# Kernel optimization log

Hardware: AMD Instinct MI355X
Metric: run time of the kernel (lower is better)

## Reference

```python
import jax, jax.numpy as jnp
from jax import lax
import numpy as np

WIN = 11
SIGMA = 1.5
C1 = 0.01 ** 2  # (K1 * data_range)^2 with data_range=1.0
C2 = 0.03 ** 2


def _gaussian_window(channels: int) -> jnp.ndarray:
    coords = np.arange(WIN, dtype=np.float32) - (WIN - 1) / 2.0
    g = np.exp(-(coords ** 2) / (2.0 * SIGMA ** 2))
    g /= g.sum()
    w2d = np.outer(g, g).astype(np.float32)  # [11,11]
    # OIHW depthwise kernel: [C, 1, 11, 11]
    return jnp.asarray(np.tile(w2d[None, None], (channels, 1, 1, 1)))


def _dwconv(x, w, channels):
    pad = WIN // 2
    return lax.conv_general_dilated(
        x, w, window_strides=(1, 1), padding=[(pad, pad), (pad, pad)],
        dimension_numbers=("NCHW", "OIHW", "NCHW"),
        feature_group_count=channels)


def setup_inputs() -> dict:
    key = jax.random.key(0)
    k1, k2 = jax.random.split(key)
    shape = (16, 3, 512, 512)
    pred = jax.random.uniform(k1, shape, dtype=jnp.float32)
    target = jax.random.uniform(k2, shape, dtype=jnp.float32)
    return {"pred": pred, "target": target}


def reference(pred, target):
    C = pred.shape[1]
    w = _gaussian_window(C).astype(pred.dtype)
    # Stack the five fields along batch so a single depthwise conv computes
    # all local windowed statistics in one pass (fused-stat formulation).
    B = pred.shape[0]
    stacked = jnp.concatenate(
        [pred, target, pred * pred, target * target, pred * target], axis=0)
    stats = _dwconv(stacked, w, C)
    mu1, mu2, e_x2, e_y2, e_xy = (
        stats[0:B], stats[B:2 * B], stats[2 * B:3 * B],
        stats[3 * B:4 * B], stats[4 * B:5 * B])
    mu1_sq = mu1 * mu1
    mu2_sq = mu2 * mu2
    mu1_mu2 = mu1 * mu2
    sigma1_sq = e_x2 - mu1_sq
    sigma2_sq = e_y2 - mu2_sq
    sigma12 = e_xy - mu1_mu2
    ssim_map = ((2.0 * mu1_mu2 + C1) * (2.0 * sigma12 + C2)) / (
        (mu1_sq + mu2_sq + C1) * (sigma1_sq + sigma2_sq + C2))
    return jnp.mean(ssim_map)  # size_average=True
```

## Files before the change

### kernel.cpp

```cpp
#include <hip/hip_runtime.h>
#include <math.h>

#define IMG   512
#define NIMG  48
#define TB    64
#define TC    32
#define SR    74
#define PITCH 77
#define STS   (TC * PITCH)
#define C1v   1.0e-4f
#define C2v   9.0e-4f

struct Win { float w[11]; };

template<bool GUARD>
__device__ __forceinline__ void phaseA_unit(
        float2* __restrict__ hs2,
        const float* __restrict__ P,
        const float* __restrict__ T,
        const Win& win, int bx, int y0, int x0, int u) {
    const int r  = u >> 3;
    const int cb = u & 7;
    const int gy = y0 - 5 + r;
    const float* __restrict__ Prow = P + (long)gy * IMG;
    const float* __restrict__ Trow = T + (long)gy * IMG;
    const bool yok = (!GUARD) || ((gy >= 0) & (gy < IMG));

    float s1[4], s2[4], q1[4], q2[4];
    #pragma unroll
    for (int i = 0; i < 4; ++i) { s1[i]=0.f; s2[i]=0.f; q1[i]=0.f; q2[i]=0.f; }

    #pragma unroll
    for (int k = 0; k < 5; ++k) {
        float4 p = make_float4(0.f, 0.f, 0.f, 0.f);
        float4 t = make_float4(0.f, 0.f, 0.f, 0.f);
        bool zero = false;
        if (GUARD)
            zero = (!yok) | ((bx == 0)  & (cb + k <= 1))
                          | ((bx == 15) & (cb + k >= 10));
        if (!zero) {
            const int gx = x0 + 4 * (cb + k - 2);
            p = *(const float4*)(Prow + gx);
            t = *(const float4*)(Trow + gx);
        }
        const float pv[4] = { p.x, p.y, p.z, p.w };
        const float tv[4] = { t.x, t.y, t.z, t.w };
        #pragma unroll
        for (int j4 = 0; j4 < 4; ++j4) {
            const int w = 4 * k + j4;
            if (w >= 3 && w <= 16) {
                const float sm = pv[j4] + tv[j4];
                const float dm = pv[j4] - tv[j4];
                const float sq = sm * sm;
                const float dq = dm * dm;
                #pragma unroll
                for (int i = 0; i < 4; ++i) {
                    const int j = w - 3 - i;
                    if (j >= 0 && j < 11) {
                        const float wj = win.w[j];
                        s1[i] += wj * sm;
                        s2[i] += wj * dm;
                        q1[i] += wj * sq;
                        q2[i] += wj * dq;
                    }
                }
            }
        }
    }
    const int ebase = (4 * cb) * PITCH + r;
    #pragma unroll
    for (int i = 0; i < 4; ++i) {
        hs2[ebase + i * PITCH]       = make_float2(s1[i], s2[i]);
        hs2[STS + ebase + i * PITCH] = make_float2(q1[i], q2[i]);
    }
}

__global__ __launch_bounds__(512, 8) void ssim_kernel(
        const float* __restrict__ pred,
        const float* __restrict__ targ,
        float* __restrict__ partial, Win win) {
    __shared__ float2 hs2[2 * STS];
    __shared__ float wavesum[8];

    const int tid = threadIdx.x;
    const int n   = blockIdx.z;
    const int by  = blockIdx.y;
    const int bx  = blockIdx.x;
    const int y0  = by * TB;
    const int x0  = bx * TC;

    const float* __restrict__ P = pred + (size_t)n * IMG * IMG;
    const float* __restrict__ T = targ + (size_t)n * IMG * IMG;

    const bool guard = (bx == 0) | (bx == 15) | (by == 0) | (by == (IMG / TB - 1));
    if (guard) {
        #pragma unroll 1
        for (int u = tid; u < SR * 8; u += 512)
            phaseA_unit<true >(hs2, P, T, win, bx, y0, x0, u);
    } else {
        #pragma unroll 1
        for (int u = tid; u < SR * 8; u += 512)
            phaseA_unit<false>(hs2, P, T, win, bx, y0, x0, u);
    }
    __syncthreads();

    const int x  = tid & 31;
    const int rg = tid >> 5;
    const int r0 = rg * 4;
    const float2* __restrict__ csd = &hs2[x * PITCH + r0];
    const float2* __restrict__ cqq = &hs2[STS + x * PITCH + r0];

    float sum[4][4];
    #pragma unroll
    for (int st = 0; st < 4; ++st)
        #pragma unroll
        for (int k = 0; k < 4; ++k) sum[st][k] = 0.f;

    #pragma unroll
    for (int m = 0; m < 14; ++m) {
        const float2 sd = csd[m];
        const float2 qq = cqq[m];
        #pragma unroll
        for (int k = 0; k < 4; ++k) {
            const int j = m - k;
            if (j >= 0 && j < 11) {
                const float wj = win.w[j];
                sum[0][k] += wj * sd.x;
                sum[1][k] += wj * sd.y;
                sum[2][k] += wj * qq.x;
                sum[3][k] += wj * qq.y;
            }
        }
    }

    float acc = 0.f;
    #pragma unroll
    for (int k = 0; k < 4; ++k) {
        const float S1 = sum[0][k];
        const float S2 = sum[1][k];
        const float Q1 = sum[2][k];
        const float Q2 = sum[3][k];
        const float s1q = S1 * S1;
        const float s2q = S2 * S2;
        const float A_  = 0.5f * (s1q + s2q);
        const float B_  = 0.5f * (s1q - s2q);
        const float sps = 0.5f * (Q1 + Q2) - A_;
        const float sxx = 0.5f * (Q1 - Q2) - B_;
        const float num = (B_ + C1v) * (sxx + C2v);
        const float den = (A_ + C1v) * (sps + C2v);
        acc += num * __builtin_amdgcn_rcpf(den);
    }

    #pragma unroll
    for (int off = 32; off > 0; off >>= 1)
        acc += __shfl_down(acc, off, 64);
    const int wv = tid >> 6;
    if ((tid & 63) == 0) wavesum[wv] = acc;
    __syncthreads();
    if (tid == 0) {
        float s = 0.f;
        #pragma unroll
        for (int i = 0; i < 8; ++i) s += wavesum[i];
        const int bid = (blockIdx.z * gridDim.y + blockIdx.y) * gridDim.x + blockIdx.x;
        partial[bid] = s;
    }
}

__global__ __launch_bounds__(512) void ssim_reduce_kernel(
        const float* __restrict__ partial,
        float* __restrict__ out,
        int nchunk4, double inv_n) {
    __shared__ double wsum[8];
    const float4* __restrict__ p4 = (const float4*)partial;
    double s = 0.0;
    #pragma unroll 1
    for (int i = threadIdx.x; i < nchunk4; i += 512) {
        const float4 v = p4[i];
        s += (double)((v.x + v.y) + (v.z + v.w));
    }
    #pragma unroll
    for (int off = 32; off > 0; off >>= 1)
        s += __shfl_down(s, off, 64);
    const int wv = threadIdx.x >> 6;
    if ((threadIdx.x & 63) == 0) wsum[wv] = s;
    __syncthreads();
    if (threadIdx.x == 0) {
        double tot = 0.0;
        #pragma unroll
        for (int i = 0; i < 8; ++i) tot += wsum[i];
        out[0] = (float)(tot * inv_n);
    }
}

extern "C" void kernel_launch(void* const* d_in, const int* in_sizes, int n_in,
                              void* d_out, int out_size, void* d_ws, size_t ws_size,
                              hipStream_t stream) {
    const float* pred = (const float*)d_in[0];
    const float* targ = (const float*)d_in[1];
    float* out     = (float*)d_out;
    float* partial = (float*)d_ws;

    Win win;
    {
        double v[11], s = 0.0;
        for (int i = 0; i < 11; ++i) {
            float d   = (float)i - 5.0f;
            float arg = -(d * d) / 4.5f;
            v[i] = exp((double)arg);
            s += v[i];
        }
        for (int i = 0; i < 11; ++i) win.w[i] = (float)(v[i] / s);
    }

    dim3 grid(IMG / TC, IMG / TB, NIMG);
    ssim_kernel<<<grid, 512, 0, stream>>>(pred, targ, partial, win);

    const int nblk = (IMG / TC) * (IMG / TB) * NIMG;
    const double inv_n = 1.0 / ((double)NIMG * IMG * IMG);
    ssim_reduce_kernel<<<1, 512, 0, stream>>>(partial, out, nblk / 4, inv_n);
}
```

Before: 55.10 us.

## Rebalance horizontal pass and split vertical pass by plane with shuffle exchange

The horizontal pass is split into a main phase where each of the 512 threads handles one of the first 64 rows. A tail phase spreads the remaining 10 halo rows over 20 lanes per wave at two output columns each, which removes the strided second loop iteration that left most threads idle. The vertical pass now has each thread handle one plane (sum/diff or squares) for 8 output rows over an 18-tap window. The partner plane is swapped in with a cross-half-wave shuffle, and each half computes the SSIM epilogue for 4 of the 8 rows. This cuts repeated vertical-window LDS reads and balances work, at the cost of shuffle traffic and more registers.

```diff
diff --git a/kernel.cpp b/kernel.cpp
--- a/kernel.cpp
+++ b/kernel.cpp
@@ -14,17 +14,17 @@
 struct Win { float w[11]; };
 
 template<bool GUARD>
-__device__ __forceinline__ void phaseA_unit(
+__device__ __forceinline__ void phaseA_main(
         float2* __restrict__ hs2,
         const float* __restrict__ P,
         const float* __restrict__ T,
-        const Win& win, int bx, int y0, int x0, int u) {
-    const int r  = u >> 3;
-    const int cb = u & 7;
+        const Win& win, int bx, int y0, int x0, int tid) {
+    const int r  = tid >> 3;
+    const int cb = tid & 7;
     const int gy = y0 - 5 + r;
     const float* __restrict__ Prow = P + (long)gy * IMG;
     const float* __restrict__ Trow = T + (long)gy * IMG;
-    const bool yok = (!GUARD) || ((gy >= 0) & (gy < IMG));
+    const bool yok = (!GUARD) || (gy >= 0);
 
     float s1[4], s2[4], q1[4], q2[4];
     #pragma unroll
@@ -75,6 +75,88 @@
     }
 }
 
+template<bool GUARD>
+__device__ __forceinline__ void phaseA_tail(
+        float2* __restrict__ hs2,
+        const float* __restrict__ P,
+        const float* __restrict__ T,
+        const Win& win, int bx, int y0, int x0, int tid) {
+    const int wv = tid >> 6;
+    const int l  = tid & 63;
+    if (l >= 20) return;
+    const int u   = wv * 20 + l;
+    const int r   = 64 + (u >> 4);
+    const int cb2 = u & 15;
+    const int cb  = cb2 >> 1;
+    const int h   = cb2 & 1;
+    const int gy  = y0 - 5 + r;
+    const float* __restrict__ Prow = P + (long)gy * IMG;
+    const float* __restrict__ Trow = T + (long)gy * IMG;
+    const bool yok = (!GUARD) || (gy < IMG);
+    const int lo = 3 - 2 * h;
+
+    float pa[16], pb[16];
+    #pragma unroll
+    for (int k = 0; k < 4; ++k) {
+        const int q = cb + h + k;
+        float4 p = make_float4(0.f, 0.f, 0.f, 0.f);
+        float4 t = make_float4(0.f, 0.f, 0.f, 0.f);
+        bool zero = false;
+        if (GUARD)
+            zero = (!yok) | ((bx == 0)  & (q <= 1))
+                          | ((bx == 15) & (q >= 10));
+        if (!zero) {
+            const int gx = x0 + 4 * (q - 2);
+            p = *(const float4*)(Prow + gx);
+            t = *(const float4*)(Trow + gx);
+        }
+        pa[4*k+0] = p.x; pa[4*k+1] = p.y; pa[4*k+2] = p.z; pa[4*k+3] = p.w;
+        pb[4*k+0] = t.x; pb[4*k+1] = t.y; pb[4*k+2] = t.z; pb[4*k+3] = t.w;
+    }
+
+    float s1[2], s2[2], q1[2], q2[2];
+    #pragma unroll
+    for (int c = 0; c < 2; ++c) { s1[c]=0.f; s2[c]=0.f; q1[c]=0.f; q2[c]=0.f; }
+    #pragma unroll
+    for (int m = 0; m < 12; ++m) {
+        const float a  = pa[lo + m];
+        const float b  = pb[lo + m];
+        const float sm = a + b;
+        const float dm = a - b;
+        const float sq = sm * sm;
+        const float dq = dm * dm;
+        #pragma unroll
+        for (int c = 0; c < 2; ++c) {
+            const int j = m - c;
+            if (j >= 0 && j < 11) {
+                const float wj = win.w[j];
+                s1[c] += wj * sm;
+                s2[c] += wj * dm;
+                q1[c] += wj * sq;
+                q2[c] += wj * dq;
+            }
+        }
+    }
+    #pragma unroll
+    for (int c = 0; c < 2; ++c) {
+        const int C = 4 * cb + 2 * h + c;
+        hs2[C * PITCH + r]       = make_float2(s1[c], s2[c]);
+        hs2[STS + C * PITCH + r] = make_float2(q1[c], q2[c]);
+    }
+}
+
+__device__ __forceinline__ float ssim_epilogue(float S1, float S2, float Q1, float Q2) {
+    const float s1q = S1 * S1;
+    const float s2q = S2 * S2;
+    const float A_  = 0.5f * (s1q + s2q);
+    const float B_  = 0.5f * (s1q - s2q);
+    const float sps = 0.5f * (Q1 + Q2) - A_;
+    const float sxx = 0.5f * (Q1 - Q2) - B_;
+    const float num = (B_ + C1v) * (sxx + C2v);
+    const float den = (A_ + C1v) * (sps + C2v);
+    return num * __builtin_amdgcn_rcpf(den);
+}
+
 __global__ __launch_bounds__(512, 8) void ssim_kernel(
         const float* __restrict__ pred,
         const float* __restrict__ targ,
@@ -94,61 +176,54 @@
 
     const bool guard = (bx == 0) | (bx == 15) | (by == 0) | (by == (IMG / TB - 1));
     if (guard) {
-        #pragma unroll 1
-        for (int u = tid; u < SR * 8; u += 512)
-            phaseA_unit<true >(hs2, P, T, win, bx, y0, x0, u);
+        phaseA_main<true >(hs2, P, T, win, bx, y0, x0, tid);
+        phaseA_tail<true >(hs2, P, T, win, bx, y0, x0, tid);
     } else {
-        #pragma unroll 1
-        for (int u = tid; u < SR * 8; u += 512)
-            phaseA_unit<false>(hs2, P, T, win, bx, y0, x0, u);
+        phaseA_main<false>(hs2, P, T, win, bx, y0, x0, tid);
+        phaseA_tail<false>(hs2, P, T, win, bx, y0, x0, tid);
     }
     __syncthreads();
 
     const int x  = tid & 31;
-    const int rg = tid >> 5;
-    const int r0 = rg * 4;
-    const float2* __restrict__ csd = &hs2[x * PITCH + r0];
-    const float2* __restrict__ cqq = &hs2[STS + x * PITCH + r0];
-
-    float sum[4][4];
-    #pragma unroll
-    for (int st = 0; st < 4; ++st)
-        #pragma unroll
-        for (int k = 0; k < 4; ++k) sum[st][k] = 0.f;
-
-    #pragma unroll
-    for (int m = 0; m < 14; ++m) {
-        const float2 sd = csd[m];
-        const float2 qq = cqq[m];
-        #pragma unroll
-        for (int k = 0; k < 4; ++k) {
+    const int pl = (tid >> 5) & 1;
+    const int ro = tid >> 6;
+    const int r0 = ro * 8;
+    const float2* __restrict__ cp = &hs2[pl * STS + x * PITCH + r0];
+
+    float A0[8], A1[8];
+    #pragma unroll
+    for (int k = 0; k < 8; ++k) { A0[k] = 0.f; A1[k] = 0.f; }
+
+    #pragma unroll
+    for (int m = 0; m < 18; ++m) {
+        const float2 v = cp[m];
+        #pragma unroll
+        for (int k = 0; k < 8; ++k) {
             const int j = m - k;
             if (j >= 0 && j < 11) {
                 const float wj = win.w[j];
-                sum[0][k] += wj * sd.x;
-                sum[1][k] += wj * sd.y;
-                sum[2][k] += wj * qq.x;
-                sum[3][k] += wj * qq.y;
+                A0[k] += wj * v.x;
+                A1[k] += wj * v.y;
             }
         }
     }
 
+    float O0[8], O1[8];
+    #pragma unroll
+    for (int k = 0; k < 8; ++k) {
+        O0[k] = __shfl_xor(A0[k], 32, 64);
+        O1[k] = __shfl_xor(A1[k], 32, 64);
+    }
+
     float acc = 0.f;
-    #pragma unroll
-    for (int k = 0; k < 4; ++k) {
-        const float S1 = sum[0][k];
-        const float S2 = sum[1][k];
-        const float Q1 = sum[2][k];
-        const float Q2 = sum[3][k];
-        const float s1q = S1 * S1;
-        const float s2q = S2 * S2;
-        const float A_  = 0.5f * (s1q + s2q);
-        const float B_  = 0.5f * (s1q - s2q);
-        const float sps = 0.5f * (Q1 + Q2) - A_;
-        const float sxx = 0.5f * (Q1 - Q2) - B_;
-        const float num = (B_ + C1v) * (sxx + C2v);
-        const float den = (A_ + C1v) * (sps + C2v);
-        acc += num * __builtin_amdgcn_rcpf(den);
+    if (pl == 0) {
+        #pragma unroll
+        for (int k = 0; k < 4; ++k)
+            acc += ssim_epilogue(A0[k], A1[k], O0[k], O1[k]);
+    } else {
+        #pragma unroll
+        for (int k = 4; k < 8; ++k)
+            acc += ssim_epilogue(O0[k], O1[k], A0[k], A1[k]);
     }
 
     #pragma unroll
```

Measured after the change: 99.66 us. 80.9% more time.

## Split vertical pass by plane across half-waves, 8 rows per thread with shuffle exchange

Applied to the files above, without the earlier changes.

The vertical Gaussian pass changes its work split. Each half-wave now handles one plane pair (sum/diff or squares) over 8 output rows instead of one thread covering both planes over 4 rows. Accumulation uses packed float2 vectors, which could map to packed FMA, and partner values come over with a cross-half-wave xor shuffle before the epilogue. This cuts redundant LDS reads of overlapping halo rows (18 loads for 8 rows instead of 28 for 4), at the cost of the shuffle traffic.

```diff
diff --git a/kernel.cpp b/kernel.cpp
--- a/kernel.cpp
+++ b/kernel.cpp
@@ -10,6 +10,8 @@
 #define STS   (TC * PITCH)
 #define C1v   1.0e-4f
 #define C2v   9.0e-4f
+
+typedef __attribute__((ext_vector_type(2))) float f2;
 
 struct Win { float w[11]; };
 
@@ -75,6 +77,18 @@
     }
 }
 
+__device__ __forceinline__ float ssim_epilogue(float S1, float S2, float Q1, float Q2) {
+    const float s1q = S1 * S1;
+    const float s2q = S2 * S2;
+    const float A_  = 0.5f * (s1q + s2q);
+    const float B_  = 0.5f * (s1q - s2q);
+    const float sps = 0.5f * (Q1 + Q2) - A_;
+    const float sxx = 0.5f * (Q1 - Q2) - B_;
+    const float num = (B_ + C1v) * (sxx + C2v);
+    const float den = (A_ + C1v) * (sps + C2v);
+    return num * __builtin_amdgcn_rcpf(den);
+}
+
 __global__ __launch_bounds__(512, 8) void ssim_kernel(
         const float* __restrict__ pred,
         const float* __restrict__ targ,
@@ -105,50 +119,43 @@
     __syncthreads();
 
     const int x  = tid & 31;
-    const int rg = tid >> 5;
-    const int r0 = rg * 4;
-    const float2* __restrict__ csd = &hs2[x * PITCH + r0];
-    const float2* __restrict__ cqq = &hs2[STS + x * PITCH + r0];
-
-    float sum[4][4];
-    #pragma unroll
-    for (int st = 0; st < 4; ++st)
-        #pragma unroll
-        for (int k = 0; k < 4; ++k) sum[st][k] = 0.f;
-
-    #pragma unroll
-    for (int m = 0; m < 14; ++m) {
-        const float2 sd = csd[m];
-        const float2 qq = cqq[m];
-        #pragma unroll
-        for (int k = 0; k < 4; ++k) {
+    const int pl = (tid >> 5) & 1;
+    const int ro = tid >> 6;
+    const int r0 = ro * 8;
+    const float2* __restrict__ cp = &hs2[pl * STS + x * PITCH + r0];
+
+    f2 sums[8];
+    #pragma unroll
+    for (int k = 0; k < 8; ++k) sums[k] = (f2)0.f;
+
+    #pragma unroll
+    for (int m = 0; m < 18; ++m) {
+        const float2 raw = cp[m];
+        f2 v; v.x = raw.x; v.y = raw.y;
+        #pragma unroll
+        for (int k = 0; k < 8; ++k) {
             const int j = m - k;
-            if (j >= 0 && j < 11) {
-                const float wj = win.w[j];
-                sum[0][k] += wj * sd.x;
-                sum[1][k] += wj * sd.y;
-                sum[2][k] += wj * qq.x;
-                sum[3][k] += wj * qq.y;
-            }
-        }
+            if (j >= 0 && j < 11)
+                sums[k] += win.w[j] * v;
+        }
+    }
+
+    float O0[8], O1[8];
+    #pragma unroll
+    for (int k = 0; k < 8; ++k) {
+        O0[k] = __shfl_xor(sums[k].x, 32, 64);
+        O1[k] = __shfl_xor(sums[k].y, 32, 64);
     }
 
     float acc = 0.f;
-    #pragma unroll
-    for (int k = 0; k < 4; ++k) {
-        const float S1 = sum[0][k];
-        const float S2 = sum[1][k];
-        const float Q1 = sum[2][k];
-        const float Q2 = sum[3][k];
-        const float s1q = S1 * S1;
-        const float s2q = S2 * S2;
-        const float A_  = 0.5f * (s1q + s2q);
-        const float B_  = 0.5f * (s1q - s2q);
-        const float sps = 0.5f * (Q1 + Q2) - A_;
-        const float sxx = 0.5f * (Q1 - Q2) - B_;
-        const float num = (B_ + C1v) * (sxx + C2v);
-        const float den = (A_ + C1v) * (sps + C2v);
-        acc += num * __builtin_amdgcn_rcpf(den);
+    if (pl == 0) {
+        #pragma unroll
+        for (int k = 0; k < 4; ++k)
+            acc += ssim_epilogue(sums[k].x, sums[k].y, O0[k], O1[k]);
+    } else {
+        #pragma unroll
+        for (int k = 4; k < 8; ++k)
+            acc += ssim_epilogue(O0[k], O1[k], sums[k].x, sums[k].y);
     }
 
     #pragma unroll
```

Result: slower. 58.98 us (+7.0%).
